# Performance work log

Measured on AMD Instinct MI355X. Metric: run time of the kernel, lower is better.

The kernel has to match this reference:

```python
import jax, jax.numpy as jnp
import numpy as np


def setup_inputs() -> dict:
    key = jax.random.key(0)
    ks = jax.random.split(key, 8)
    B, Cin, H, W = 4, 256, 64, 64
    Ck = Cin // 2            # 128, KAN in/out dim
    NC = 21                  # num_classes
    return {
        "x": jax.random.normal(ks[0], (B, Cin, H, W), dtype=jnp.float32),
        "conv1_w": jax.random.normal(ks[1], (Ck, Cin, 3, 3), dtype=jnp.float32) * 0.02,
        "conv1_b": jnp.zeros((Ck,), dtype=jnp.float32),
        "kan_scale": jnp.ones((Ck, Ck), dtype=jnp.float32)
                     + 0.1 * jax.random.normal(ks[2], (Ck, Ck), dtype=jnp.float32),
        "kan_translation": 0.1 * jax.random.normal(ks[3], (Ck, Ck), dtype=jnp.float32),
        "kan_wavelet_weight": jax.random.normal(ks[4], (Ck, Ck), dtype=jnp.float32) * 0.1,
        "kan_base_weight": jax.random.normal(ks[5], (Ck, Ck), dtype=jnp.float32) * 0.05,
        "conv2_w": jax.random.normal(ks[6], (NC, Ck, 1, 1), dtype=jnp.float32) * 0.05,
        "conv2_b": jnp.zeros((NC,), dtype=jnp.float32),
    }


def _conv2d(x, w, b, pad):
    y = jax.lax.conv_general_dilated(
        x, w, window_strides=(1, 1), padding=pad,
        dimension_numbers=("NCHW", "OIHW", "NCHW"))
    return y + b[None, :, None, None]


def _wavelet_kan(x, scale, translation, wav_w, base_w):
    # x: (N, Cin). Wav-KAN (DoG) layer:
    #   u = (x - translation) / scale, per (out, in) pair -> (N, O, I)
    #   dog(u) = -u * exp(-u^2 / 2)
    #   wavelet_out[n, o] = sum_i dog(u)[n, o, i] * wav_w[o, i]
    #   base_out = silu(x) @ base_w.T
    u = (x[:, None, :] - translation[None]) / scale[None]          # (N, O, I)
    dog = -u * jnp.exp(-0.5 * u * u)                               # (N, O, I)
    wav_out = jnp.einsum("noi,oi->no", dog, wav_w)                 # (N, O)
    base_out = jnp.einsum("ni,oi->no", jax.nn.silu(x), base_w)     # (N, O)
    return wav_out + base_out


def reference(x, conv1_w, conv1_b, kan_scale, kan_translation,
              kan_wavelet_weight, kan_base_weight, conv2_w, conv2_b):
    h = jax.nn.relu(_conv2d(x, conv1_w, conv1_b, ((1, 1), (1, 1))))   # (B, Ck, H, W)
    B, C, H, W = h.shape
    flat = h.transpose(0, 2, 3, 1).reshape(B * H * W, C)              # (N, Ck)
    k = _wavelet_kan(flat, kan_scale, kan_translation,
                     kan_wavelet_weight, kan_base_weight)             # (N, Ck)
    k = k.reshape(B, H, W, -1).transpose(0, 3, 1, 2)                  # (B, Ck, H, W)
    return _conv2d(k, conv2_w, conv2_b, ((0, 0), (0, 0)))             # (B, NC, H, W)
```

## Files before the change

### kernel.cpp

```cpp
#include <hip/hip_runtime.h>
#include <math.h>

typedef __attribute__((ext_vector_type(8))) short s16x8;
typedef __attribute__((ext_vector_type(4))) float f32x4;
typedef __attribute__((ext_vector_type(2))) float f32x2;

#define LOG2E 1.4426950408889634f

#define OFF_XH   0
#define OFF_WB   2097152
#define OFF_PQT  2244608
#define OFF_W2   2310144
#define OFF_H    2315520

__global__ __launch_bounds__(256) void prep_all_k(
    const float* __restrict__ x, const float* __restrict__ w1,
    const float* __restrict__ ks, const float* __restrict__ kt,
    const float* __restrict__ kw, const float* __restrict__ kb,
    const float* __restrict__ w2, float* __restrict__ ws) {
  int blk = blockIdx.x;
  int t = threadIdx.x;
  if (blk < 1024) {
    __shared__ float lsm[64][65];
    unsigned short* xh = (unsigned short*)(ws + OFF_XH);
    int pr = blk & 63, cib = (blk >> 6) & 3, bb = blk >> 8;
    int sp0 = pr * 64;
    const float* src = x + (unsigned)(bb * 256 + cib * 64) * 4096 + sp0;
#pragma unroll
    for (int rr = 0; rr < 16; ++rr) {
      int idx = rr * 256 + t;
      int ci = idx >> 6, px = idx & 63;
      lsm[ci][px] = src[ci * 4096 + px];
    }
    __syncthreads();
#pragma unroll
    for (int rr = 0; rr < 16; ++rr) {
      int idx = rr * 256 + t;
      int px = idx >> 6, ci = idx & 63;
      unsigned u = __float_as_uint(lsm[ci][px]);
      xh[(unsigned)(bb * 4096 + sp0 + px) * 256 + cib * 64 + ci] =
          (unsigned short)((u + 0x7FFF + ((u >> 16) & 1)) >> 16);
    }
  } else if (blk < 2251) {
    int tid = (blk - 1024) * 256 + t;
    unsigned short* Wb = (unsigned short*)(ws + OFF_WB);
    if (tid < 294912) {
      int j = tid & 7, co = (tid >> 3) & 63, g = (tid >> 9) & 3, r = tid >> 11;
      int t9 = r % 9, q = r / 9, ck = q & 7, chh = q >> 3;
      int ci = ck * 32 + g * 8 + j, cog = chh * 64 + co;
      unsigned u = __float_as_uint(w1[(unsigned)(cog * 256 + ci) * 9 + t9]);
      Wb[tid] = (unsigned short)((u + 0x7FFF + ((u >> 16) & 1)) >> 16);
    } else if (tid < 294912 + 16384) {
      int i2 = tid - 294912;
      int i = i2 >> 7, o = i2 & 127;
      int ic = i >> 3, k = i & 7;
      float rs = 1.f / ks[o * 128 + i];
      float T  = kt[o * 128 + i];
      float A  = -0.7213475204444817f * rs * rs;
      float Bq = -2.f * A * T;
      float C  = A * T * T;
      float P0 = -rs * kw[o * 128 + i];
      float sc = exp2f(C);
      int khi = k >> 2, klo = k & 3;
      unsigned base = ((unsigned)ic * 8 * 128 + o) * 4 + klo;
      ws[OFF_PQT + base + (0 + khi) * 512] = A;
      ws[OFF_PQT + base + (2 + khi) * 512] = Bq;
      ws[OFF_PQT + base + (4 + khi) * 512] = P0 * sc;
      ws[OFF_PQT + base + (6 + khi) * 512] = -P0 * T * sc;
    } else if (tid < 294912 + 16384 + 2688) {
      int i3 = tid - 294912 - 16384;
      int nc = i3 >> 7, k = i3 & 127;
      ws[OFF_W2 + nc * 256 + k] = w2[nc * 128 + k];
    }
  } else {
    int nc = blk - 2251;
    if (t < 128) {
      float acc = 0.f;
      for (int o = 0; o < 128; ++o)
        acc = fmaf(w2[nc * 128 + o], kb[o * 128 + t], acc);
      ws[OFF_W2 + nc * 256 + 128 + t] = acc;
    }
  }
}

__global__ __launch_bounds__(256, 2) void conv1_mfma_k(
    const unsigned short* __restrict__ xh, const unsigned short* __restrict__ Wb,
    const float* __restrict__ b1, float* __restrict__ h) {
  __shared__ unsigned short Asm[3 * 66 * 40];
  __shared__ unsigned short Bsm[18432];
  int blk = blockIdx.x;
  int ch = blk & 1, y = (blk >> 1) & 63, bb = blk >> 7;
  int t = threadIdx.x;
  int wave = t >> 6, lane = t & 63;
  int wx = wave & 1, wn = wave >> 1;
  int l15 = lane & 15, lg = lane >> 4;

  if (t < 6) {
    int r = t >> 1, xl = (t & 1) * 65;
    float4 z = {0, 0, 0, 0};
    float4* p = (float4*)&Asm[(r * 66 + xl) * 40];
    p[0] = z; p[1] = z; p[2] = z; p[3] = z; p[4] = z;
  }

  f32x4 acc[2][2];
  f32x4 zz = {0.f, 0.f, 0.f, 0.f};
  acc[0][0] = zz; acc[0][1] = zz; acc[1][0] = zz; acc[1][1] = zz;

  int r_st = t >> 6, x_st = t & 63;
  int gy = y - 1 + r_st;
  bool arow = (r_st < 3);
  bool yok = arow & (gy >= 0) & (gy < 64);
  const unsigned short* asrc = xh + (unsigned)(bb * 4096 + gy * 64 + x_st) * 256;
  unsigned short* adst = &Asm[(r_st * 66 + x_st + 1) * 40];
  const unsigned short* bslab = Wb + ch * 8 * 18432;

  for (int ck = 0; ck < 8; ++ck) {
    float4 v0 = {0, 0, 0, 0}, v1 = v0, v2 = v0, v3 = v0;
    if (yok) {
      const float4* s = (const float4*)(asrc + ck * 32);
      v0 = s[0]; v1 = s[1]; v2 = s[2]; v3 = s[3];
    }
    if (arow) { float4* d = (float4*)adst; d[0] = v0; d[1] = v1; d[2] = v2; d[3] = v3; }
    {
      const float4* s = (const float4*)(bslab + ck * 18432);
      float4* d = (float4*)Bsm;
#pragma unroll
      for (int j = 0; j < 9; ++j) d[j * 256 + t] = s[j * 256 + t];
    }
    __syncthreads();
#pragma unroll
    for (int t9 = 0; t9 < 9; ++t9) {
      int ky = t9 / 3, kx = t9 % 3;
      s16x8 a[2], b[2];
      int abase = (ky * 66 + wx * 32 + l15 + kx) * 40 + lg * 8;
#pragma unroll
      for (int f = 0; f < 2; ++f)
        a[f] = *(const s16x8*)&Asm[abase + f * 640];
#pragma unroll
      for (int n = 0; n < 2; ++n)
        b[n] = *(const s16x8*)&Bsm[((t9 * 4 + lg) * 64 + wn * 32 + n * 16 + l15) * 8];
#pragma unroll
      for (int f = 0; f < 2; ++f)
#pragma unroll
        for (int n = 0; n < 2; ++n)
          acc[f][n] = __builtin_amdgcn_mfma_f32_16x16x32_bf16(a[f], b[n], acc[f][n], 0, 0, 0);
    }
    __syncthreads();
  }
#pragma unroll
  for (int n = 0; n < 2; ++n) {
    int co = ch * 64 + wn * 32 + n * 16 + l15;
    float bz = b1[co];
#pragma unroll
    for (int f = 0; f < 2; ++f) {
      int xbase = wx * 32 + f * 16 + lg * 4;
      float* dst = h + (unsigned)(bb * 4096 + y * 64 + xbase) * 128 + co;
#pragma unroll
      for (int r = 0; r < 4; ++r) {
        float v = acc[f][n][r] + bz;
        dst[r * 128] = v > 0.f ? v : 0.f;
      }
    }
  }
}

__global__ __launch_bounds__(256) void wavkan_k(
    const float* __restrict__ h, const float* __restrict__ PQT,
    float* __restrict__ kwout) {
  __shared__ float hsm[8][128];
  __shared__ f32x2 red[2][8][64];
  int n0 = blockIdx.x * 8;
  int t = threadIdx.x;
  {
    int row = t >> 5, c4 = (t & 31) * 4;
    *(float4*)&hsm[row][c4] = *(const float4*)&h[(unsigned)(n0 + row) * 128 + c4];
  }
  __syncthreads();

  int wave = t >> 6, lane = t & 63;
  int ich = wave & 1;
  int oh  = wave >> 1;
  int o   = oh * 64 + lane;

  f32x2 accv[8];
#pragma unroll
  for (int n = 0; n < 8; ++n) accv[n] = (f32x2){0.f, 0.f};

  const float4* pq = (const float4*)PQT + o;

  for (int ic = ich * 8; ic < ich * 8 + 8; ++ic) {
    const float4* pp = pq + (unsigned)ic * 1024;
    float4 r0 = pp[0],   r1 = pp[128], r2 = pp[256], r3 = pp[384],
           r4 = pp[512], r5 = pp[640], r6 = pp[768], r7 = pp[896];
    f32x2 A2[4] = {{r0.x, r0.y}, {r0.z, r0.w}, {r1.x, r1.y}, {r1.z, r1.w}};
    f32x2 B2[4] = {{r2.x, r2.y}, {r2.z, r2.w}, {r3.x, r3.y}, {r3.z, r3.w}};
    f32x2 P2[4] = {{r4.x, r4.y}, {r4.z, r4.w}, {r5.x, r5.y}, {r5.z, r5.w}};
    f32x2 D2[4] = {{r6.x, r6.y}, {r6.z, r6.w}, {r7.x, r7.y}, {r7.z, r7.w}};
    int i0 = ic * 8;
#pragma unroll
    for (int n = 0; n < 8; ++n) {
      float4 h0 = *(const float4*)&hsm[n][i0];
      float4 h1 = *(const float4*)&hsm[n][i0 + 4];
      f32x2 hh[4] = {{h0.x, h0.y}, {h0.z, h0.w}, {h1.x, h1.y}, {h1.z, h1.w}};
      f32x2 a2 = accv[n];
#pragma unroll
      for (int q = 0; q < 4; ++q) {
        f32x2 h2 = hh[q];
        f32x2 t2 = A2[q] * h2 + B2[q];
        f32x2 u2 = t2 * h2;
        f32x2 e2;
        e2.x = __builtin_amdgcn_exp2f(u2.x);
        e2.y = __builtin_amdgcn_exp2f(u2.y);
        f32x2 v2 = P2[q] * h2 + D2[q];
        a2 = v2 * e2 + a2;
      }
      accv[n] = a2;
    }
  }

  if (ich) {
#pragma unroll
    for (int n = 0; n < 8; ++n) red[oh][n][lane] = accv[n];
  }
  __syncthreads();
  if (!ich) {
#pragma unroll
    for (int n = 0; n < 8; ++n) {
      f32x2 r = red[oh][n][lane];
      kwout[(unsigned)(n0 + n) * 128 + o] =
          (accv[n].x + r.x) + (accv[n].y + r.y);
    }
  }
}

__global__ __launch_bounds__(256) void conv2_k(
    const float* __restrict__ kwv, const float* __restrict__ h,
    const float* __restrict__ w2c, const float* __restrict__ b2,
    float* __restrict__ out) {
  __shared__ float ksm[32][260];
  __shared__ float wsm[21 * 256];
  int n0 = blockIdx.x * 32;
  int t = threadIdx.x;
#pragma unroll 2
  for (int rr = 0; rr < 4; ++rr) {
    int idx4 = rr * 256 + t;
    int row = idx4 >> 5, c4 = (idx4 & 31) * 4;
    *(float4*)&ksm[row][c4] = *(const float4*)&kwv[(unsigned)(n0 + row) * 128 + c4];
    float4 v = *(const float4*)&h[(unsigned)(n0 + row) * 128 + c4];
    float4 s;
    s.x = v.x * __builtin_amdgcn_rcpf(1.f + __builtin_amdgcn_exp2f(-LOG2E * v.x));
    s.y = v.y * __builtin_amdgcn_rcpf(1.f + __builtin_amdgcn_exp2f(-LOG2E * v.y));
    s.z = v.z * __builtin_amdgcn_rcpf(1.f + __builtin_amdgcn_exp2f(-LOG2E * v.z));
    s.w = v.w * __builtin_amdgcn_rcpf(1.f + __builtin_amdgcn_exp2f(-LOG2E * v.w));
    *(float4*)&ksm[row][128 + c4] = s;
  }
#pragma unroll 2
  for (int j = t; j < 1344; j += 256)
    *(float4*)&wsm[j * 4] = *(const float4*)&w2c[j * 4];
  __syncthreads();

  int n = t & 31, ncg = t >> 5;
  float a0 = 0.f, a1 = 0.f, a2 = 0.f;
  bool has2 = ncg < 5;
#pragma unroll 4
  for (int i4 = 0; i4 < 64; ++i4) {
    float4 k4 = *(const float4*)&ksm[n][i4 * 4];
    float4 wA = *(const float4*)&wsm[ncg * 256 + i4 * 4];
    float4 wB = *(const float4*)&wsm[(ncg + 8) * 256 + i4 * 4];
    a0 += k4.x * wA.x + k4.y * wA.y + k4.z * wA.z + k4.w * wA.w;
    a1 += k4.x * wB.x + k4.y * wB.y + k4.z * wB.z + k4.w * wB.w;
    if (has2) {
      float4 wC = *(const float4*)&wsm[(ncg + 16) * 256 + i4 * 4];
      a2 += k4.x * wC.x + k4.y * wC.y + k4.z * wC.z + k4.w * wC.w;
    }
  }
  int gn = n0 + n, bb = gn >> 12, sp = gn & 4095;
  out[(unsigned)(bb * 21 + ncg) * 4096 + sp] = a0 + b2[ncg];
  out[(unsigned)(bb * 21 + ncg + 8) * 4096 + sp] = a1 + b2[ncg + 8];
  if (has2) out[(unsigned)(bb * 21 + ncg + 16) * 4096 + sp] = a2 + b2[ncg + 16];
}

extern "C" void kernel_launch(void* const* d_in, const int* in_sizes, int n_in,
                              void* d_out, int out_size, void* d_ws, size_t ws_size,
                              hipStream_t stream) {
  const float* x  = (const float*)d_in[0];
  const float* w1 = (const float*)d_in[1];
  const float* b1 = (const float*)d_in[2];
  const float* ks = (const float*)d_in[3];
  const float* kt = (const float*)d_in[4];
  const float* kw = (const float*)d_in[5];
  const float* kb = (const float*)d_in[6];
  const float* w2 = (const float*)d_in[7];
  const float* b2 = (const float*)d_in[8];
  float* out = (float*)d_out;
  float* ws  = (float*)d_ws;

  prep_all_k<<<2272, 256, 0, stream>>>(x, w1, ks, kt, kw, kb, w2, ws);
  conv1_mfma_k<<<512, 256, 0, stream>>>((const unsigned short*)(ws + OFF_XH),
                                        (const unsigned short*)(ws + OFF_WB),
                                        b1, ws + OFF_H);
  wavkan_k<<<2048, 256, 0, stream>>>(ws + OFF_H, ws + OFF_PQT,
                                     ws + OFF_XH );
  conv2_k<<<512, 256, 0, stream>>>(ws + OFF_XH, ws + OFF_H, ws + OFF_W2, b2, out);
}
```

Measured before the change: 90.75 us.

## Fuse wavelet-KAN and 1x1 conv2 into a single kernel

Merges the wavelet-KAN kernel with the conv2 kernel so the per-pixel KAN output stays in shared memory instead of round-tripping through global workspace. The silu of h is computed in place from the already-staged tile, and 168 threads compute the 21-class outputs for 8 pixels by reading the folded conv2 weights directly from global/L2. This removes one launch and the write and reread of the KAN intermediate. In exchange, most threads sit idle in the conv2 tail, weights are reread per block without LDS staging, and output stores are narrower.

```diff
diff --git a/kernel.cpp b/kernel.cpp
--- a/kernel.cpp
+++ b/kernel.cpp
@@ -164,11 +164,13 @@
   }
 }
 
-__global__ __launch_bounds__(256) void wavkan_k(
+__global__ __launch_bounds__(256) void wavkan_conv2_k(
     const float* __restrict__ h, const float* __restrict__ PQT,
-    float* __restrict__ kwout) {
-  __shared__ float hsm[8][128];
+    const float* __restrict__ w2c, const float* __restrict__ b2,
+    float* __restrict__ out) {
+  __shared__ float hsm[8][132];
   __shared__ f32x2 red[2][8][64];
+  __shared__ float ksm[8][132];
   int n0 = blockIdx.x * 8;
   int t = threadIdx.x;
   {
@@ -227,57 +229,42 @@
 #pragma unroll
     for (int n = 0; n < 8; ++n) {
       f32x2 r = red[oh][n][lane];
-      kwout[(unsigned)(n0 + n) * 128 + o] =
-          (accv[n].x + r.x) + (accv[n].y + r.y);
-    }
-  }
-}
-
-__global__ __launch_bounds__(256) void conv2_k(
-    const float* __restrict__ kwv, const float* __restrict__ h,
-    const float* __restrict__ w2c, const float* __restrict__ b2,
-    float* __restrict__ out) {
-  __shared__ float ksm[32][260];
-  __shared__ float wsm[21 * 256];
-  int n0 = blockIdx.x * 32;
-  int t = threadIdx.x;
-#pragma unroll 2
-  for (int rr = 0; rr < 4; ++rr) {
-    int idx4 = rr * 256 + t;
-    int row = idx4 >> 5, c4 = (idx4 & 31) * 4;
-    *(float4*)&ksm[row][c4] = *(const float4*)&kwv[(unsigned)(n0 + row) * 128 + c4];
-    float4 v = *(const float4*)&h[(unsigned)(n0 + row) * 128 + c4];
+      ksm[n][o] = (accv[n].x + r.x) + (accv[n].y + r.y);
+    }
+  }
+  {
+    int n = t >> 5, c4 = (t & 31) * 4;
+    float4 v = *(float4*)&hsm[n][c4];
     float4 s;
     s.x = v.x * __builtin_amdgcn_rcpf(1.f + __builtin_amdgcn_exp2f(-LOG2E * v.x));
     s.y = v.y * __builtin_amdgcn_rcpf(1.f + __builtin_amdgcn_exp2f(-LOG2E * v.y));
     s.z = v.z * __builtin_amdgcn_rcpf(1.f + __builtin_amdgcn_exp2f(-LOG2E * v.z));
     s.w = v.w * __builtin_amdgcn_rcpf(1.f + __builtin_amdgcn_exp2f(-LOG2E * v.w));
-    *(float4*)&ksm[row][128 + c4] = s;
-  }
-#pragma unroll 2
-  for (int j = t; j < 1344; j += 256)
-    *(float4*)&wsm[j * 4] = *(const float4*)&w2c[j * 4];
+    *(float4*)&hsm[n][c4] = s;
+  }
   __syncthreads();
 
-  int n = t & 31, ncg = t >> 5;
-  float a0 = 0.f, a1 = 0.f, a2 = 0.f;
-  bool has2 = ncg < 5;
+  if (t < 168) {
+    int n = t & 7, g = t >> 3;
+    const float* w0 = w2c + g * 256;
+    const float* kr = &ksm[n][0];
+    const float* hr = &hsm[n][0];
+    float a0 = 0.f;
 #pragma unroll 4
-  for (int i4 = 0; i4 < 64; ++i4) {
-    float4 k4 = *(const float4*)&ksm[n][i4 * 4];
-    float4 wA = *(const float4*)&wsm[ncg * 256 + i4 * 4];
-    float4 wB = *(const float4*)&wsm[(ncg + 8) * 256 + i4 * 4];
-    a0 += k4.x * wA.x + k4.y * wA.y + k4.z * wA.z + k4.w * wA.w;
-    a1 += k4.x * wB.x + k4.y * wB.y + k4.z * wB.z + k4.w * wB.w;
-    if (has2) {
-      float4 wC = *(const float4*)&wsm[(ncg + 16) * 256 + i4 * 4];
-      a2 += k4.x * wC.x + k4.y * wC.y + k4.z * wC.z + k4.w * wC.w;
-    }
-  }
-  int gn = n0 + n, bb = gn >> 12, sp = gn & 4095;
-  out[(unsigned)(bb * 21 + ncg) * 4096 + sp] = a0 + b2[ncg];
-  out[(unsigned)(bb * 21 + ncg + 8) * 4096 + sp] = a1 + b2[ncg + 8];
-  if (has2) out[(unsigned)(bb * 21 + ncg + 16) * 4096 + sp] = a2 + b2[ncg + 16];
+    for (int k4 = 0; k4 < 32; ++k4) {
+      float4 kv = *(const float4*)&kr[k4 * 4];
+      float4 w = *(const float4*)&w0[k4 * 4];
+      a0 += kv.x * w.x + kv.y * w.y + kv.z * w.z + kv.w * w.w;
+    }
+#pragma unroll 4
+    for (int k4 = 0; k4 < 32; ++k4) {
+      float4 hv = *(const float4*)&hr[k4 * 4];
+      float4 w = *(const float4*)&w0[128 + k4 * 4];
+      a0 += hv.x * w.x + hv.y * w.y + hv.z * w.z + hv.w * w.w;
+    }
+    int gn = n0 + n, bb = gn >> 12, sp = gn & 4095;
+    out[(unsigned)(bb * 21 + g) * 4096 + sp] = a0 + b2[g];
+  }
 }
 
 extern "C" void kernel_launch(void* const* d_in, const int* in_sizes, int n_in,
@@ -299,7 +286,6 @@
   conv1_mfma_k<<<512, 256, 0, stream>>>((const unsigned short*)(ws + OFF_XH),
                                         (const unsigned short*)(ws + OFF_WB),
                                         b1, ws + OFF_H);
-  wavkan_k<<<2048, 256, 0, stream>>>(ws + OFF_H, ws + OFF_PQT,
-                                     ws + OFF_XH );
-  conv2_k<<<512, 256, 0, stream>>>(ws + OFF_XH, ws + OFF_H, ws + OFF_W2, b2, out);
-}
+  wavkan_conv2_k<<<2048, 256, 0, stream>>>(ws + OFF_H, ws + OFF_PQT,
+                                           ws + OFF_W2, b2, out);
+}
```

New measurement: 84.85 us. -6.5%, faster.
